# Kernel tuning notes

Measured on AMD Instinct MI355X. Metric: run time of the kernel, lower is better.

The kernel has to match this reference:

```python
import jax, jax.numpy as jnp
import numpy as np

B, S, D, H = 4, 2048, 512, 8
HD = D // H  # head_dim = 64


def setup_inputs() -> dict:
    key = jax.random.key(0)
    ks = jax.random.split(key, 10)
    scale = 1.0 / np.sqrt(D)  # keep activations O(1)
    x = jax.random.normal(ks[0], (B, S, D), dtype=jnp.float32)
    # causal mask, broadcast over batch and heads
    causal = jnp.tril(jnp.ones((S, S), dtype=bool))
    mask = jnp.broadcast_to(causal, (B, H, S, S))
    def lin(k):
        return jax.random.normal(k, (D, D), dtype=jnp.float32) * scale
    return {
        "x": x,
        "mask": mask,
        "Wq": lin(ks[1]), "bq": jax.random.normal(ks[2], (D,), dtype=jnp.float32) * 0.01,
        "Wk": lin(ks[3]), "bk": jax.random.normal(ks[4], (D,), dtype=jnp.float32) * 0.01,
        "Wv": lin(ks[5]), "bv": jax.random.normal(ks[6], (D,), dtype=jnp.float32) * 0.01,
        "Wo": lin(ks[7]), "bo": jax.random.normal(ks[8], (D,), dtype=jnp.float32) * 0.01,
    }


def reference(x, mask, Wq, bq, Wk, bk, Wv, bv, Wo, bo):
    # eqx.nn.Linear computes W @ x + b per row; batched form is x @ W.T + b.
    b, s, d = x.shape
    q = jnp.einsum("bsd,ed->bse", x, Wq) + bq
    k = jnp.einsum("bsd,ed->bse", x, Wk) + bk
    v = jnp.einsum("bsd,ed->bse", x, Wv) + bv
    # [B, H, S, HD]
    q = q.reshape(b, s, H, HD).transpose(0, 2, 1, 3)
    k = k.reshape(b, s, H, HD).transpose(0, 2, 1, 3)
    v = v.reshape(b, s, H, HD).transpose(0, 2, 1, 3)
    scores = jnp.einsum("bhqd,bhkd->bhqk", q, k) / jnp.sqrt(jnp.asarray(HD, x.dtype))
    scores = jnp.where(mask, scores, jnp.asarray(-1e9, x.dtype))
    attn = jax.nn.softmax(scores, axis=-1)
    attended = jnp.einsum("bhqk,bhkd->bhqd", attn, v)
    attended = attended.transpose(0, 2, 1, 3).reshape(b, s, d)
    out = jnp.einsum("bsd,ed->bse", attended, Wo) + bo
    return out
```

## Files before the change

### kernel.cpp

```cpp
#include <hip/hip_runtime.h>

#define S_LEN 2048
#define DM    512
#define NH    8
#define HD    64

typedef unsigned short u16;
typedef unsigned int   u32;
typedef __bf16 bf16_t;
typedef bf16_t bf16x8 __attribute__((ext_vector_type(8)));
typedef float  f32x4  __attribute__((ext_vector_type(4)));

__device__ __forceinline__ u16 f2bf(float f) {
    u32 u = __float_as_uint(f);
    u += 0x7FFFu + ((u >> 16) & 1u);
    return (u16)(u >> 16);
}

__device__ __forceinline__ void g2l16(const u16* g, u16* l) {
    __builtin_amdgcn_global_load_lds(
        (const __attribute__((address_space(1))) u32*)g,
        (__attribute__((address_space(3))) u32*)l,
        16, 0, 0);
}

__device__ __forceinline__ float qmax16(float v) {
    v = fmaxf(v, __shfl_xor(v, 1));
    v = fmaxf(v, __shfl_xor(v, 2));
    v = fmaxf(v, __shfl_xor(v, 4));
    v = fmaxf(v, __shfl_xor(v, 8));
    return v;
}
__device__ __forceinline__ float qsum16(float v) {
    v += __shfl_xor(v, 1);
    v += __shfl_xor(v, 2);
    v += __shfl_xor(v, 4);
    v += __shfl_xor(v, 8);
    return v;
}

__global__ __launch_bounds__(256) void cvt_bf16(
    const float* __restrict__ x,
    const float* __restrict__ wq, const float* __restrict__ wk,
    const float* __restrict__ wv, const float* __restrict__ wo,
    u16* __restrict__ xb, u16* __restrict__ wqb, u16* __restrict__ wkb,
    u16* __restrict__ wvb, u16* __restrict__ wob)
{
    const int y = blockIdx.y;
    const float* src; u16* dst; int n;
    if (y == 0)      { src = x;  dst = xb;  n = 4 * S_LEN * DM; }
    else if (y == 1) { src = wq; dst = wqb; n = DM * DM; }
    else if (y == 2) { src = wk; dst = wkb; n = DM * DM; }
    else if (y == 3) { src = wv; dst = wvb; n = DM * DM; }
    else             { src = wo; dst = wob; n = DM * DM; }
    int idx = (blockIdx.x * 256 + threadIdx.x) * 8;
    if (idx >= n) return;
    float4 f0 = *(const float4*)(src + idx);
    float4 f1 = *(const float4*)(src + idx + 4);
    u32 p0 = (u32)f2bf(f0.x) | ((u32)f2bf(f0.y) << 16);
    u32 p1 = (u32)f2bf(f0.z) | ((u32)f2bf(f0.w) << 16);
    u32 p2 = (u32)f2bf(f1.x) | ((u32)f2bf(f1.y) << 16);
    u32 p3 = (u32)f2bf(f1.z) | ((u32)f2bf(f1.w) << 16);
    *(uint4*)(dst + idx) = make_uint4(p0, p1, p2, p3);
}

__global__ __launch_bounds__(256) void qkv_gemm(
    const u16* __restrict__ xb,
    const u16* __restrict__ Wqb, const u16* __restrict__ Wkb, const u16* __restrict__ Wvb,
    const float* __restrict__ bq, const float* __restrict__ bk, const float* __restrict__ bv,
    u16* __restrict__ Qb, u16* __restrict__ Kb, u16* __restrict__ Vb)
{
    __shared__ u16 Als[2][4096];
    __shared__ u16 Bls[2][4096];

    const int t = threadIdx.x;
    const int lane = t & 63, w = t >> 6;
    const int ln = lane & 15, quad = lane >> 4;
    const int wm = w >> 1, wn = w & 1;
    const int m0 = blockIdx.x * 128;
    const int mat = blockIdx.y >> 2;
    const int n0 = (blockIdx.y & 3) * 128;

    const u16* __restrict__ Wb     = (mat == 0) ? Wqb : (mat == 1) ? Wkb : Wvb;
    const float* __restrict__ bias = (mat == 0) ? bq : (mat == 1) ? bk : bv;
    u16* __restrict__ outp         = (mat == 0) ? Qb : (mat == 1) ? Kb : Vb;
    const float qscale             = (mat == 0) ? 0.18033688f : 1.0f;

    const int ch0 = (w * 2 + 0) * 64 + lane;
    const int ch1 = (w * 2 + 1) * 64 + lane;
    const int sr0 = ch0 >> 2, sk0 = (ch0 & 3) ^ ((sr0 >> 1) & 3);
    const int sr1 = ch1 >> 2, sk1 = (ch1 & 3) ^ ((sr1 >> 1) & 3);
    const u16* pA0 = xb + (size_t)(m0 + sr0) * DM + sk0 * 8;
    const u16* pA1 = xb + (size_t)(m0 + sr1) * DM + sk1 * 8;
    const u16* pB0 = Wb + (size_t)(n0 + sr0) * DM + sk0 * 8;
    const u16* pB1 = Wb + (size_t)(n0 + sr1) * DM + sk1 * 8;
    const int lo0 = (w * 2 + 0) * 512;
    const int lo1 = (w * 2 + 1) * 512;

    g2l16(pA0, &Als[0][lo0]);
    g2l16(pA1, &Als[0][lo1]);
    g2l16(pB0, &Bls[0][lo0]);
    g2l16(pB1, &Bls[0][lo1]);

    f32x4 acc[4][4] = {};
    for (int it = 0; it < 16; ++it) {
        const int cur = it & 1, nxt = cur ^ 1;
        __syncthreads();
        if (it + 1 < 16) {
            const int k0n = (it + 1) * 32;
            g2l16(pA0 + k0n, &Als[nxt][lo0]);
            g2l16(pA1 + k0n, &Als[nxt][lo1]);
            g2l16(pB0 + k0n, &Bls[nxt][lo0]);
            g2l16(pB1 + k0n, &Bls[nxt][lo1]);
        }
        bf16x8 af[4], bf8[4];
        #pragma unroll
        for (int i = 0; i < 4; ++i) {
            int row = wm * 64 + i * 16 + ln;
            af[i] = *(const bf16x8*)(&Als[cur][0] + (row * 4 + (quad ^ ((row >> 1) & 3))) * 8);
        }
        #pragma unroll
        for (int j = 0; j < 4; ++j) {
            int row = wn * 64 + j * 16 + ln;
            bf8[j] = *(const bf16x8*)(&Bls[cur][0] + (row * 4 + (quad ^ ((row >> 1) & 3))) * 8);
        }
        #pragma unroll
        for (int i = 0; i < 4; ++i)
            #pragma unroll
            for (int j = 0; j < 4; ++j)
                acc[i][j] = __builtin_amdgcn_mfma_f32_16x16x32_bf16(af[i], bf8[j], acc[i][j], 0, 0, 0);
    }

    #pragma unroll
    for (int j = 0; j < 4; ++j) {
        int colg = n0 + wn * 64 + j * 16 + ln;
        float bj = bias[colg];
        int h = colg >> 6, d = colg & 63;
        #pragma unroll
        for (int i = 0; i < 4; ++i) {
            int mbase = m0 + wm * 64 + i * 16 + quad * 4;
            #pragma unroll
            for (int r = 0; r < 4; ++r) {
                int m = mbase + r;
                int bb = m >> 11, s = m & 2047;
                float v = (acc[i][j][r] + bj) * qscale;
                if (mat == 2) {
                    outp[(((size_t)bb * NH + h) * HD + d) * S_LEN + s] = f2bf(v);
                } else {
                    outp[(((size_t)bb * NH + h) * S_LEN + s) * HD + d] = f2bf(v);
                }
            }
        }
    }
}

__global__ __launch_bounds__(256) void attn_mfma(
    const u16* __restrict__ Qb, const u16* __restrict__ Kb, const u16* __restrict__ Vb,
    u16* __restrict__ Attb)
{
    __shared__ u16 Qls[4096];
    __shared__ u16 Kls[2][4096];
    __shared__ u16 Vt[2][4096];
    __shared__ u16 Ps[4096];

    const int t = threadIdx.x;
    const int lane = t & 63, w = t >> 6;
    const int ln = lane & 15, quad = lane >> 4;
    const int bh = blockIdx.y;
    const int qt = (blockIdx.x + bh) & 31;
    const int q_base = qt * 64;
    const size_t base = (size_t)bh * S_LEN * HD;

    const int c0 = (w * 2 + 0) * 64 + lane;
    const int c1 = (w * 2 + 1) * 64 + lane;
    const int r0 = c0 >> 3, k0s = (c0 & 7) ^ (r0 & 7);
    const int r1 = c1 >> 3, k1s = (c1 & 7) ^ (r1 & 7);
    const int lo0 = (w * 2 + 0) * 512;
    const int lo1 = (w * 2 + 1) * 512;

    g2l16(Qb + base + (size_t)(q_base + r0) * HD + k0s * 8, Qls + lo0);
    g2l16(Qb + base + (size_t)(q_base + r1) * HD + k1s * 8, Qls + lo1);

    const u16* pK0 = Kb + base + (size_t)r0 * HD + k0s * 8;
    const u16* pK1 = Kb + base + (size_t)r1 * HD + k1s * 8;
    g2l16(pK0, &Kls[0][lo0]);
    g2l16(pK1, &Kls[0][lo1]);

    const u16* pV0 = Vb + base + (size_t)r0 * S_LEN + k0s * 8;
    const u16* pV1 = Vb + base + (size_t)r1 * S_LEN + k1s * 8;
    g2l16(pV0, &Vt[0][lo0]);
    g2l16(pV1, &Vt[0][lo1]);

    __syncthreads();

    bf16x8 aq[2];
    #pragma unroll
    for (int ks = 0; ks < 2; ++ks) {
        int row = w * 16 + ln;
        aq[ks] = *(const bf16x8*)(Qls + (row * 8 + ((ks * 4 + quad) ^ (row & 7))) * 8);
    }

    float m_st[4], l_st[4], alpha[4];
    f32x4 o[4] = {};
    #pragma unroll
    for (int r = 0; r < 4; ++r) { m_st[r] = -1e30f; l_st[r] = 0.f; }

    const int qrow_base = q_base + w * 16;

    for (int kt = 0; kt <= qt; ++kt) {
        const int cur = kt & 1, nxt = cur ^ 1;
        __syncthreads();

        if (kt < qt) {
            const size_t offK = (size_t)(kt + 1) * 64 * HD;
            const size_t offV = (size_t)(kt + 1) * 64;
            g2l16(pK0 + offK, &Kls[nxt][lo0]);
            g2l16(pK1 + offK, &Kls[nxt][lo1]);
            g2l16(pV0 + offV, &Vt[nxt][lo0]);
            g2l16(pV1 + offV, &Vt[nxt][lo1]);
        }

        f32x4 s[4] = {};
        #pragma unroll
        for (int ks = 0; ks < 2; ++ks)
            #pragma unroll
            for (int j = 0; j < 4; ++j) {
                int krow = j * 16 + ln;
                bf16x8 bk8 = *(const bf16x8*)(&Kls[cur][0] + (krow * 8 + ((ks * 4 + quad) ^ (krow & 7))) * 8);
                s[j] = __builtin_amdgcn_mfma_f32_16x16x32_bf16(aq[ks], bk8, s[j], 0, 0, 0);
            }

        if (kt == qt) {
            #pragma unroll
            for (int j = 0; j < 4; ++j)
                #pragma unroll
                for (int r = 0; r < 4; ++r) {
                    int qg = qrow_base + quad * 4 + r;
                    int kg = kt * 64 + j * 16 + ln;
                    if (kg > qg) s[j][r] = -1e30f;
                }
        }

        #pragma unroll
        for (int r = 0; r < 4; ++r) {
            float mx = fmaxf(fmaxf(s[0][r], s[1][r]), fmaxf(s[2][r], s[3][r]));
            mx = qmax16(mx);
            float mnew = fmaxf(m_st[r], mx);
            float al = __builtin_amdgcn_exp2f(m_st[r] - mnew);
            m_st[r] = mnew;
            float rs = 0.f;
            #pragma unroll
            for (int j = 0; j < 4; ++j) {
                float p = __builtin_amdgcn_exp2f(s[j][r] - mnew);
                s[j][r] = p;
                rs += p;
            }
            rs = qsum16(rs);
            l_st[r] = l_st[r] * al + rs;
            alpha[r] = al;
        }
        #pragma unroll
        for (int j = 0; j < 4; ++j)
            #pragma unroll
            for (int r = 0; r < 4; ++r)
                o[j][r] *= alpha[r];

        #pragma unroll
        for (int j = 0; j < 4; ++j) {
            int key = j * 16 + ln;
            int kq = key >> 3, kl = key & 7;
            #pragma unroll
            for (int r = 0; r < 4; ++r) {
                int qrow = w * 16 + quad * 4 + r;
                Ps[(qrow * 8 + (kq ^ (qrow & 7))) * 8 + kl] = f2bf(s[j][r]);
            }
        }

        #pragma unroll
        for (int ks = 0; ks < 2; ++ks) {
            int prow = w * 16 + ln;
            bf16x8 pa = *(const bf16x8*)(Ps + (prow * 8 + ((ks * 4 + quad) ^ (prow & 7))) * 8);
            #pragma unroll
            for (int j = 0; j < 4; ++j) {
                int rowd = j * 16 + ln;
                bf16x8 vb8 = *(const bf16x8*)(&Vt[cur][0] + (rowd * 8 + ((ks * 4 + quad) ^ (rowd & 7))) * 8);
                o[j] = __builtin_amdgcn_mfma_f32_16x16x32_bf16(pa, vb8, o[j], 0, 0, 0);
            }
        }
    }

    const int bb = bh >> 3, h = bh & 7;
    #pragma unroll
    for (int r = 0; r < 4; ++r) {
        int qg = q_base + w * 16 + quad * 4 + r;
        float inv = 1.f / l_st[r];
        #pragma unroll
        for (int j = 0; j < 4; ++j) {
            int d = j * 16 + ln;
            Attb[((size_t)(bb * S_LEN + qg)) * DM + h * HD + d] = f2bf(o[j][r] * inv);
        }
    }
}

__global__ __launch_bounds__(256) void out_gemm(
    const u16* __restrict__ Ab, const u16* __restrict__ Wob,
    const float* __restrict__ bo, float* __restrict__ out)
{
    __shared__ u16 Als[2][2048];
    __shared__ u16 Bls[2][4096];

    const int t = threadIdx.x;
    const int lane = t & 63, w = t >> 6;
    const int ln = lane & 15, quad = lane >> 4;
    const int m0 = blockIdx.x * 64;
    const int n0 = blockIdx.y * 128;

    const int cha = w * 64 + lane;
    const int sra = cha >> 2, ska = (cha & 3) ^ ((sra >> 1) & 3);
    const u16* pA = Ab + (size_t)(m0 + sra) * DM + ska * 8;
    const int loa = w * 512;

    const int ch0 = (w * 2 + 0) * 64 + lane;
    const int ch1 = (w * 2 + 1) * 64 + lane;
    const int sr0 = ch0 >> 2, sk0 = (ch0 & 3) ^ ((sr0 >> 1) & 3);
    const int sr1 = ch1 >> 2, sk1 = (ch1 & 3) ^ ((sr1 >> 1) & 3);
    const u16* pB0 = Wob + (size_t)(n0 + sr0) * DM + sk0 * 8;
    const u16* pB1 = Wob + (size_t)(n0 + sr1) * DM + sk1 * 8;
    const int lo0 = (w * 2 + 0) * 512;
    const int lo1 = (w * 2 + 1) * 512;

    g2l16(pA,  &Als[0][loa]);
    g2l16(pB0, &Bls[0][lo0]);
    g2l16(pB1, &Bls[0][lo1]);

    f32x4 acc[4][2] = {};
    for (int it = 0; it < 16; ++it) {
        const int cur = it & 1, nxt = cur ^ 1;
        __syncthreads();
        if (it + 1 < 16) {
            const int k0n = (it + 1) * 32;
            g2l16(pA + k0n,  &Als[nxt][loa]);
            g2l16(pB0 + k0n, &Bls[nxt][lo0]);
            g2l16(pB1 + k0n, &Bls[nxt][lo1]);
        }
        bf16x8 af[4], bf8[2];
        #pragma unroll
        for (int i = 0; i < 4; ++i) {
            int row = i * 16 + ln;
            af[i] = *(const bf16x8*)(&Als[cur][0] + (row * 4 + (quad ^ ((row >> 1) & 3))) * 8);
        }
        #pragma unroll
        for (int j = 0; j < 2; ++j) {
            int row = w * 32 + j * 16 + ln;
            bf8[j] = *(const bf16x8*)(&Bls[cur][0] + (row * 4 + (quad ^ ((row >> 1) & 3))) * 8);
        }
        #pragma unroll
        for (int i = 0; i < 4; ++i)
            #pragma unroll
            for (int j = 0; j < 2; ++j)
                acc[i][j] = __builtin_amdgcn_mfma_f32_16x16x32_bf16(af[i], bf8[j], acc[i][j], 0, 0, 0);
    }

    #pragma unroll
    for (int j = 0; j < 2; ++j) {
        int colg = n0 + w * 32 + j * 16 + ln;
        float bj = bo[colg];
        #pragma unroll
        for (int i = 0; i < 4; ++i) {
            int mbase = m0 + i * 16 + quad * 4;
            #pragma unroll
            for (int r = 0; r < 4; ++r) {
                int m = mbase + r;
                out[(size_t)m * DM + colg] = acc[i][j][r] + bj;
            }
        }
    }
}

extern "C" void kernel_launch(void* const* d_in, const int* in_sizes, int n_in,
                              void* d_out, int out_size, void* d_ws, size_t ws_size,
                              hipStream_t stream) {
    const float* x  = (const float*)d_in[0];
    const float* Wq = (const float*)d_in[2];
    const float* bq = (const float*)d_in[3];
    const float* Wk = (const float*)d_in[4];
    const float* bk = (const float*)d_in[5];
    const float* Wv = (const float*)d_in[6];
    const float* bv = (const float*)d_in[7];
    const float* Wo = (const float*)d_in[8];
    const float* bo = (const float*)d_in[9];
    float* out = (float*)d_out;

    u16* ws = (u16*)d_ws;
    const size_t NX = (size_t)4 * S_LEN * DM;
    const size_t NW = (size_t)DM * DM;
    u16* xb   = ws;
    u16* wqb  = xb + NX;
    u16* wkb  = wqb + NW;
    u16* wvb  = wkb + NW;
    u16* wob  = wvb + NW;
    u16* Qb   = wob + NW;
    u16* Kb   = Qb + NX;
    u16* Vb   = Kb + NX;
    u16* Attb = Vb + NX;

    cvt_bf16<<<dim3(2048, 5), 256, 0, stream>>>(x, Wq, Wk, Wv, Wo, xb, wqb, wkb, wvb, wob);
    qkv_gemm<<<dim3(64, 12), 256, 0, stream>>>(xb, wqb, wkb, wvb, bq, bk, bv, Qb, Kb, Vb);
    attn_mfma<<<dim3(32, 32), 256, 0, stream>>>(Qb, Kb, Vb, Attb);
    out_gemm<<<dim3(128, 4), 256, 0, stream>>>(Attb, wob, bo, out);
}
```

Measured before the change: 735.1 us.

## Enlarge attention query tile to 128 rows with 8 waves sharing K/V tiles

The attention kernel now processes 128 query rows per block using 512 threads (8 waves), so each K/V tile loaded into LDS is reused by twice as many waves. Each thread issues one K and one V async load per tile instead of two, and the grid halves to 16x32 blocks. The causal mask is applied to the last two key tiles. The cost is fewer blocks, coarser load balance across the causal triangle, and more LDS per block; waves on the lower half of the query tile also process a key tile that is fully masked for them.

```diff
diff --git a/kernel.cpp b/kernel.cpp
--- a/kernel.cpp
+++ b/kernel.cpp
@@ -154,42 +154,39 @@
     }
 }
 
-__global__ __launch_bounds__(256) void attn_mfma(
+__global__ __launch_bounds__(512, 4) void attn_mfma(
     const u16* __restrict__ Qb, const u16* __restrict__ Kb, const u16* __restrict__ Vb,
     u16* __restrict__ Attb)
 {
-    __shared__ u16 Qls[4096];
+    __shared__ u16 Qls[8192];
     __shared__ u16 Kls[2][4096];
     __shared__ u16 Vt[2][4096];
-    __shared__ u16 Ps[4096];
+    __shared__ u16 Ps[8192];
 
     const int t = threadIdx.x;
     const int lane = t & 63, w = t >> 6;
     const int ln = lane & 15, quad = lane >> 4;
     const int bh = blockIdx.y;
-    const int qt = (blockIdx.x + bh) & 31;
-    const int q_base = qt * 64;
+    const int qt = (blockIdx.x + bh) & 15;
+    const int q_base = qt * 128;
     const size_t base = (size_t)bh * S_LEN * HD;
 
-    const int c0 = (w * 2 + 0) * 64 + lane;
-    const int c1 = (w * 2 + 1) * 64 + lane;
-    const int r0 = c0 >> 3, k0s = (c0 & 7) ^ (r0 & 7);
-    const int r1 = c1 >> 3, k1s = (c1 & 7) ^ (r1 & 7);
-    const int lo0 = (w * 2 + 0) * 512;
-    const int lo1 = (w * 2 + 1) * 512;
-
-    g2l16(Qb + base + (size_t)(q_base + r0) * HD + k0s * 8, Qls + lo0);
-    g2l16(Qb + base + (size_t)(q_base + r1) * HD + k1s * 8, Qls + lo1);
-
-    const u16* pK0 = Kb + base + (size_t)r0 * HD + k0s * 8;
-    const u16* pK1 = Kb + base + (size_t)r1 * HD + k1s * 8;
-    g2l16(pK0, &Kls[0][lo0]);
-    g2l16(pK1, &Kls[0][lo1]);
-
-    const u16* pV0 = Vb + base + (size_t)r0 * S_LEN + k0s * 8;
-    const u16* pV1 = Vb + base + (size_t)r1 * S_LEN + k1s * 8;
-    g2l16(pV0, &Vt[0][lo0]);
-    g2l16(pV1, &Vt[0][lo1]);
+    const int rK = t >> 3, kKs = (t & 7) ^ (rK & 7);
+    const int loK = w * 512;
+
+    {
+        const int c0 = t, c1 = t + 512;
+        const int qr0 = c0 >> 3, qk0 = (c0 & 7) ^ (qr0 & 7);
+        const int qr1 = c1 >> 3, qk1 = (c1 & 7) ^ (qr1 & 7);
+        g2l16(Qb + base + (size_t)(q_base + qr0) * HD + qk0 * 8, Qls + w * 512);
+        g2l16(Qb + base + (size_t)(q_base + qr1) * HD + qk1 * 8, Qls + 4096 + w * 512);
+    }
+
+    const u16* pK = Kb + base + (size_t)rK * HD + kKs * 8;
+    g2l16(pK, &Kls[0][loK]);
+
+    const u16* pV = Vb + base + (size_t)rK * S_LEN + kKs * 8;
+    g2l16(pV, &Vt[0][loK]);
 
     __syncthreads();
 
@@ -206,18 +203,15 @@
     for (int r = 0; r < 4; ++r) { m_st[r] = -1e30f; l_st[r] = 0.f; }
 
     const int qrow_base = q_base + w * 16;
-
-    for (int kt = 0; kt <= qt; ++kt) {
+    const int ktmax = 2 * qt + 1;
+
+    for (int kt = 0; kt <= ktmax; ++kt) {
         const int cur = kt & 1, nxt = cur ^ 1;
         __syncthreads();
 
-        if (kt < qt) {
-            const size_t offK = (size_t)(kt + 1) * 64 * HD;
-            const size_t offV = (size_t)(kt + 1) * 64;
-            g2l16(pK0 + offK, &Kls[nxt][lo0]);
-            g2l16(pK1 + offK, &Kls[nxt][lo1]);
-            g2l16(pV0 + offV, &Vt[nxt][lo0]);
-            g2l16(pV1 + offV, &Vt[nxt][lo1]);
+        if (kt < ktmax) {
+            g2l16(pK + (size_t)(kt + 1) * 64 * HD, &Kls[nxt][loK]);
+            g2l16(pV + (size_t)(kt + 1) * 64,      &Vt[nxt][loK]);
         }
 
         f32x4 s[4] = {};
@@ -230,7 +224,7 @@
                 s[j] = __builtin_amdgcn_mfma_f32_16x16x32_bf16(aq[ks], bk8, s[j], 0, 0, 0);
             }
 
-        if (kt == qt) {
+        if (kt >= 2 * qt) {
             #pragma unroll
             for (int j = 0; j < 4; ++j)
                 #pragma unroll
@@ -406,6 +400,6 @@
 
     cvt_bf16<<<dim3(2048, 5), 256, 0, stream>>>(x, Wq, Wk, Wv, Wo, xb, wqb, wkb, wvb, wob);
     qkv_gemm<<<dim3(64, 12), 256, 0, stream>>>(xb, wqb, wkb, wvb, bq, bk, bv, Qb, Kb, Vb);
-    attn_mfma<<<dim3(32, 32), 256, 0, stream>>>(Qb, Kb, Vb, Attb);
+    attn_mfma<<<dim3(16, 32), 512, 0, stream>>>(Qb, Kb, Vb, Attb);
     out_gemm<<<dim3(128, 4), 256, 0, stream>>>(Attb, wob, bo, out);
 }
```

Result: no change. 727.7 us (-1.0%).
